# Kernel optimization log

Measured on AMD Instinct MI355X. Metric: run time of the kernel, lower is better.

Reference implementation:

```python
import jax, jax.numpy as jnp
import numpy as np

B, V, E = 8, 12288, 98304   # batch, nodes (healpix nside=32), edges (~8 nbrs/node)
FIN, FOUT, K = 256, 256, 4  # channels, Chebyshev order
EPS = 1e-5                  # BatchNorm1d eps


def setup_inputs() -> dict:
    key = jax.random.key(0)
    ks = jax.random.split(key, 5)
    x = jax.random.normal(ks[0], (B, V, FIN), jnp.float32)
    edge_src = jax.random.randint(ks[1], (E,), 0, V, dtype=jnp.int32)
    edge_dst = jax.random.randint(ks[2], (E,), 0, V, dtype=jnp.int32)
    edge_weight = jax.random.normal(ks[3], (E,), jnp.float32) * 0.3
    scale = (2.0 / (FIN * K)) ** 0.5  # kaiming-style init over K*Fin fan-in
    weight = jax.random.normal(ks[4], (K, FIN, FOUT), jnp.float32) * scale
    bias = jnp.zeros((FOUT,), jnp.float32)
    gamma = jnp.ones((FOUT,), jnp.float32)
    beta = jnp.zeros((FOUT,), jnp.float32)
    return {"x": x, "edge_weight": edge_weight, "weight": weight, "bias": bias,
            "gamma": gamma, "beta": beta, "edge_src": edge_src, "edge_dst": edge_dst}


def reference(x, edge_weight, weight, bias, gamma, beta, edge_src, edge_dst):
    # --- ConvCheb: Chebyshev polynomial recursion over sparse Laplacian ---
    xt = x.transpose(1, 0, 2)  # [V, B, Fin] (node-major for segment scatter)

    def lmul(y):  # sparse L @ y, y: [V, B, Fin]
        msg = edge_weight[:, None, None] * y[edge_src]          # [E, B, Fin]
        return jax.ops.segment_sum(msg, edge_dst, num_segments=V)

    xs = [xt]                                  # T_0(L) x = x
    if K > 1:
        xs.append(lmul(xt))                    # T_1(L) x = L x
    for _ in range(2, K):
        xs.append(2.0 * lmul(xs[-1]) - xs[-2])  # T_k = 2 L T_{k-1} - T_{k-2}
    xk = jnp.stack(xs)                         # [K, V, B, Fin]

    out = jnp.einsum('kvbi,kio->bvo', xk, weight) + bias  # [B, V, Fout]

    # --- BatchNorm1d over channels (training-mode batch stats over B,V) ---
    mean = out.mean(axis=(0, 1))
    var = out.var(axis=(0, 1))  # biased variance, as torch uses for normalization
    out = gamma * (out - mean) * jax.lax.rsqrt(var + EPS) + beta

    return jax.nn.relu(out)
```

## Files before the change

kernel.cpp:

```cpp
#include <hip/hip_runtime.h>

#define Vn    12288
#define En    98304
#define Mrows 98304

typedef unsigned short u16;
typedef u16   u16x8  __attribute__((ext_vector_type(8)));
typedef __bf16 bf16x8 __attribute__((ext_vector_type(8)));
typedef float f32x4  __attribute__((ext_vector_type(4)));

struct __align__(8) Edge { int s; float w; };

__device__ __forceinline__ float bf2f(u16 u) {
    union { float f; unsigned int i; } c; c.i = ((unsigned int)u) << 16; return c.f;
}
__device__ __forceinline__ u16 f2bf(float f) {
    union { float f; unsigned int i; } c; c.f = f;
    unsigned int r = c.i + 0x7fffu + ((c.i >> 16) & 1u);
    return (u16)(r >> 16);
}
__device__ __forceinline__ void load_lds16(const void* g, void* l) {
    __builtin_amdgcn_global_load_lds(
        (const __attribute__((address_space(1))) void*)g,
        (__attribute__((address_space(3))) void*)l, 16, 0, 0);
}

__global__ void cvt_k(const float* __restrict__ x, u16* __restrict__ xb) {
    int v = blockIdx.x;
    int t = threadIdx.x;
    int b = t >> 5, i = (t & 31) * 8;
    const float* p = x + ((size_t)b * Vn + v) * 256 + i;
    f32x4 a0 = __builtin_nontemporal_load((const f32x4*)p);
    f32x4 a1 = __builtin_nontemporal_load((const f32x4*)(p + 4));
    u16x8 r;
    #pragma unroll
    for (int j = 0; j < 4; ++j) { r[j] = f2bf(a0[j]); r[4 + j] = f2bf(a1[j]); }
    *(u16x8*)(xb + (size_t)v * 2048 + b * 256 + i) = r;
}

__global__ void wtrans_k(const float* __restrict__ w, u16* __restrict__ wt) {
    __shared__ u16 tile[32][1026];
    int o0 = blockIdx.x * 32;
    int t  = threadIdx.x;
    int lo = t & 31;
    int kr = t >> 5;
    for (int kk0 = 0; kk0 < 1024; kk0 += 8) {
        int kk = kk0 + kr;
        tile[lo][kk] = f2bf(w[(size_t)kk * 256 + o0 + lo]);
    }
    __syncthreads();
    for (int i = 0; i < 16; ++i) {
        int ch = i * 256 + t;
        int r = ch >> 7, c = ch & 127;
        u16x8 vv = *(const u16x8*)(&tile[r][c * 8]);
        *(u16x8*)(wt + (size_t)(o0 + r) * 1024 + c * 8) = vv;
    }
}

__global__ void count_k(const int* __restrict__ dst, int* __restrict__ counts) {
    int e = blockIdx.x * 256 + threadIdx.x;
    atomicAdd(&counts[dst[e]], 1);
}

__global__ void scan_k(const int* __restrict__ counts, int* __restrict__ row_start,
                       int* __restrict__ cursor) {
    __shared__ int par[1024];
    int t = threadIdx.x;
    int base = t * 12;
    int s = 0;
    #pragma unroll
    for (int i = 0; i < 12; ++i) s += counts[base + i];
    par[t] = s;
    __syncthreads();
    for (int off = 1; off < 1024; off <<= 1) {
        int v_ = (t >= off) ? par[t - off] : 0;
        __syncthreads();
        par[t] += v_;
        __syncthreads();
    }
    int run = (t == 0) ? 0 : par[t - 1];
    for (int i = 0; i < 12; ++i) {
        row_start[base + i] = run;
        cursor[base + i]    = run;
        run += counts[base + i];
    }
    if (t == 1023) row_start[Vn] = En;
}

__global__ void fill_k(const int* __restrict__ src, const int* __restrict__ dst,
                       const float* __restrict__ ew, int* __restrict__ cursor,
                       Edge* __restrict__ csr) {
    int e = blockIdx.x * 256 + threadIdx.x;
    int d = dst[e];
    int p = atomicAdd(&cursor[d], 1);
    Edge ed; ed.s = src[e]; ed.w = ew[e];
    csr[p] = ed;
}

template<int PREV>
__global__ __launch_bounds__(256)
void lmul_k(const u16* __restrict__ yb, const u16* __restrict__ prevb,
            u16* __restrict__ outb, const int* __restrict__ row_start,
            const Edge* __restrict__ csr)
{
    int slice = blockIdx.x & 7;
    int v     = (blockIdx.x >> 3) * 8 + (threadIdx.x >> 5);
    int t     = threadIdx.x & 31;
    int s0    = row_start[v];
    int cnt   = row_start[v + 1] - s0;
    size_t soff = (size_t)slice * 256 + (size_t)t * 8;
    float acc[8] = {0.f,0.f,0.f,0.f,0.f,0.f,0.f,0.f};
    for (int j0 = 0; j0 < cnt; j0 += 8) {
        int ss[8]; float ww[8];
        #pragma unroll
        for (int u = 0; u < 8; ++u) {
            int j = j0 + u;
            bool ok = j < cnt;
            Edge e = csr[s0 + (ok ? j : 0)];
            ss[u] = e.s; ww[u] = ok ? e.w : 0.f;
        }
        u16x8 g[8];
        #pragma unroll
        for (int u = 0; u < 8; ++u)
            g[u] = *(const u16x8*)(yb + (size_t)ss[u] * 2048 + soff);
        #pragma unroll
        for (int u = 0; u < 8; ++u)
            #pragma unroll
            for (int j8 = 0; j8 < 8; ++j8) acc[j8] += ww[u] * bf2f(g[u][j8]);
    }
    u16x8 r;
    if (PREV) {
        u16x8 pu = *(const u16x8*)(prevb + (size_t)v * 2048 + soff);
        #pragma unroll
        for (int j8 = 0; j8 < 8; ++j8) r[j8] = f2bf(2.0f * acc[j8] - bf2f(pu[j8]));
    } else {
        #pragma unroll
        for (int j8 = 0; j8 < 8; ++j8) r[j8] = f2bf(acc[j8]);
    }
    *(u16x8*)(outb + (size_t)v * 2048 + soff) = r;
}

__device__ __forceinline__ void stage_tile(const u16* __restrict__ Ak, int k0,
                                           const u16* __restrict__ wt, int kt,
                                           int m0, int tid, int wave,
                                           char* bufA, char* bufB)
{
    #pragma unroll
    for (int r = 0; r < 2; ++r) {
        int g  = r * 512 + tid;
        int ml = g >> 3;
        int c  = (g & 7) ^ (ml & 7);
        load_lds16(Ak + ((size_t)(m0 + ml)) * 256 + k0 + c * 8,
                   bufA + r * 8192 + wave * 1024);
    }
    #pragma unroll
    for (int r = 0; r < 4; ++r) {
        int g = r * 512 + tid;
        int o = g >> 3;
        int c = (g & 7) ^ (o & 7);
        load_lds16(wt + (size_t)o * 1024 + kt * 64 + c * 8,
                   bufB + r * 8192 + wave * 1024);
    }
}

__global__ __launch_bounds__(512)
void gemm_k(const u16* __restrict__ x0, const u16* __restrict__ x1,
            const u16* __restrict__ x2, const u16* __restrict__ x3,
            const u16* __restrict__ wt, const float* __restrict__ bias,
            u16* cbp, float* __restrict__ sums, float* __restrict__ sumsq)
{
    alignas(16) __shared__ char lds[147456];
    int tid  = threadIdx.x;
    int wave = tid >> 6;
    int lane = tid & 63;
    int m0   = blockIdx.x * 128;
    int wm   = wave & 1;
    int wn   = wave >> 1;

    f32x4 acc[4][4];
    #pragma unroll
    for (int a = 0; a < 4; ++a)
        #pragma unroll
        for (int b = 0; b < 4; ++b) acc[a][b] = (f32x4){0.f,0.f,0.f,0.f};

    stage_tile(x0, 0,  wt, 0, m0, tid, wave, (char*)lds,         (char*)lds + 16384);
    stage_tile(x0, 64, wt, 1, m0, tid, wave, (char*)lds + 49152, (char*)lds + 49152 + 16384);

    int cb = 0;
    int pb = 2;
    for (int t = 0; t < 16; ++t) {
        if (t < 15) asm volatile("s_waitcnt vmcnt(6) lgkmcnt(0)" ::: "memory");
        else        asm volatile("s_waitcnt vmcnt(0) lgkmcnt(0)" ::: "memory");
        __builtin_amdgcn_s_barrier();
        __builtin_amdgcn_sched_barrier(0);
        if (t < 14) {
            int kt = t + 2;
            int ks = kt >> 2;
            int k0 = (kt & 3) * 64;
            const u16* Ak = (ks == 0) ? x0 : (ks == 1) ? x1 : (ks == 2) ? x2 : x3;
            stage_tile(Ak, k0, wt, kt, m0, tid, wave,
                       (char*)lds + pb * 49152, (char*)lds + pb * 49152 + 16384);
        }
        const char* Ab = (const char*)lds + cb * 49152;
        const char* Bb = Ab + 16384;
        #pragma unroll
        for (int kstep = 0; kstep < 2; ++kstep) {
            int cidx = kstep * 4 + (lane >> 4);
            int row  = lane & 15;
            bf16x8 af[4], bfr[4];
            #pragma unroll
            for (int mt = 0; mt < 4; ++mt) {
                int m16 = wm * 64 + mt * 16 + row;
                af[mt] = *(const bf16x8*)(Ab + (size_t)(m16 * 8 + (cidx ^ (m16 & 7))) * 16);
            }
            #pragma unroll
            for (int nt = 0; nt < 4; ++nt) {
                int ol = wn * 64 + nt * 16 + row;
                bfr[nt] = *(const bf16x8*)(Bb + (size_t)(ol * 8 + (cidx ^ (ol & 7))) * 16);
            }
            __builtin_amdgcn_s_setprio(1);
            #pragma unroll
            for (int mt = 0; mt < 4; ++mt)
                #pragma unroll
                for (int nt = 0; nt < 4; ++nt)
                    acc[mt][nt] = __builtin_amdgcn_mfma_f32_16x16x32_bf16(
                        af[mt], bfr[nt], acc[mt][nt], 0, 0, 0);
            __builtin_amdgcn_s_setprio(0);
        }
        cb = (cb == 2) ? 0 : cb + 1;
        pb = (pb == 2) ? 0 : pb + 1;
    }

    __syncthreads();
    int crow = lane & 15, quad = lane >> 4;
    #pragma unroll
    for (int nt = 0; nt < 4; ++nt) {
        int o = wn * 64 + nt * 16 + crow;
        int c_o = o >> 3, o_in = (o & 7) * 2;
        float bv = bias[o];
        float ps = 0.f, pq = 0.f;
        #pragma unroll
        for (int mt = 0; mt < 4; ++mt) {
            #pragma unroll
            for (int r = 0; r < 4; ++r) {
                int ml = wm * 64 + mt * 16 + quad * 4 + r;
                u16 q = f2bf(acc[mt][nt][r] + bv);
                float vq = bf2f(q);
                *(u16*)(lds + (size_t)ml * 512 + (size_t)(c_o ^ (ml & 7)) * 16 + o_in) = q;
                ps += vq; pq += vq * vq;
            }
        }
        ps += __shfl_down(ps, 32, 64);  pq += __shfl_down(pq, 32, 64);
        ps += __shfl_down(ps, 16, 64);  pq += __shfl_down(pq, 16, 64);
        if (quad == 0) { atomicAdd(&sums[o], ps); atomicAdd(&sumsq[o], pq); }
    }
    __syncthreads();
    #pragma unroll
    for (int rr = 0; rr < 8; ++rr) {
        int ch = rr * 512 + tid;
        int ml = ch >> 5, c = ch & 31;
        u16x8 vv = *(const u16x8*)(lds + (size_t)ml * 512 + (size_t)(c ^ (ml & 7)) * 16);
        *(u16x8*)(cbp + (size_t)(m0 + ml) * 256 + c * 8) = vv;
    }
}

__global__ void bn_relu_k(const u16* __restrict__ cb, float* __restrict__ outp,
                          const float* __restrict__ sums, const float* __restrict__ sumsq,
                          const float* __restrict__ gamma, const float* __restrict__ beta) {
    __shared__ float ssc[256], ssh[256];
    int t = threadIdx.x;
    {
        const float invM = 1.0f / (float)Mrows;
        float mean = sums[t] * invM;
        float var  = sumsq[t] * invM - mean * mean;
        float sc   = gamma[t] * rsqrtf(var + 1e-5f);
        ssc[t] = sc;
        ssh[t] = beta[t] - mean * sc;
    }
    __syncthreads();
    size_t p = ((size_t)blockIdx.x * 256 + t) * 8;
    int o0 = (int)(p & 255);
    int m  = (int)(p >> 8);
    u16x8 v = __builtin_nontemporal_load((const u16x8*)(cb + p));
    float* dst = outp + ((size_t)((m & 7) * Vn + (m >> 3))) * 256 + o0;
    f32x4 a, c;
    #pragma unroll
    for (int i = 0; i < 4; ++i) {
        a[i] = fmaxf(bf2f(v[i])     * ssc[o0 + i]     + ssh[o0 + i],     0.f);
        c[i] = fmaxf(bf2f(v[4 + i]) * ssc[o0 + 4 + i] + ssh[o0 + 4 + i], 0.f);
    }
    __builtin_nontemporal_store(a, (f32x4*)dst);
    __builtin_nontemporal_store(c, (f32x4*)(dst + 4));
}

extern "C" void kernel_launch(void* const* d_in, const int* in_sizes, int n_in,
                              void* d_out, int out_size, void* d_ws, size_t ws_size,
                              hipStream_t stream) {
    const float* x     = (const float*)d_in[0];
    const float* ew    = (const float*)d_in[1];
    const float* w     = (const float*)d_in[2];
    const float* bias  = (const float*)d_in[3];
    const float* gamma = (const float*)d_in[4];
    const float* beta  = (const float*)d_in[5];
    const int*   esrc  = (const int*)d_in[6];
    const int*   edst  = (const int*)d_in[7];
    float* outp = (float*)d_out;
    char*  ws   = (char*)d_ws;

    u16*   xb        = (u16*)  (ws + 0);
    u16*   x1        = (u16*)  (ws + 50331648);
    u16*   x2        = (u16*)  (ws + 100663296);
    u16*   x3        = (u16*)  (ws + 150994944);
    u16*   wt        = (u16*)  (ws + 201326592);
    Edge*  csr       = (Edge*) (ws + 201850880);
    int*   counts    = (int*)  (ws + 202637312);
    int*   row_start = (int*)  (ws + 202686464);
    int*   cursor    = (int*)  (ws + 202736128);
    float* sums      = (float*)(ws + 202785280);
    float* sumsq     = (float*)(ws + 202786304);

    hipMemsetAsync(counts, 0, 49152, stream);
    hipMemsetAsync(sums, 0, 2048, stream);

    cvt_k<<<Vn, 256, 0, stream>>>(x, xb);
    wtrans_k<<<8, 256, 0, stream>>>(w, wt);
    count_k<<<384, 256, 0, stream>>>(edst, counts);
    scan_k<<<1, 1024, 0, stream>>>(counts, row_start, cursor);
    fill_k<<<384, 256, 0, stream>>>(esrc, edst, ew, cursor, csr);

    lmul_k<0><<<Vn, 256, 0, stream>>>(xb, nullptr, x1, row_start, csr);
    lmul_k<1><<<Vn, 256, 0, stream>>>(x1, xb,      x2, row_start, csr);
    lmul_k<1><<<Vn, 256, 0, stream>>>(x2, x1,      x3, row_start, csr);

    gemm_k<<<Mrows / 128, 512, 0, stream>>>(xb, x1, x2, x3, wt, bias,
                                            (u16*)x1, sums, sumsq);

    bn_relu_k<<<12288, 256, 0, stream>>>((const u16*)x1, outp, sums, sumsq, gamma, beta);
}
```

Before: 467.0 us.

## Fuse BatchNorm+ReLU into persistent GEMM kernel with a grid-wide barrier

The GEMM becomes persistent: 256 blocks each process three 128-row tiles and accumulate the channel sums as before. An atomic counter then acts as a grid-wide barrier, after which each block computes the BN scale and shift and applies BN+ReLU to its own tiles. This drops the separate bn_relu launch and lets the BN phase read its bf16 tiles while they are likely still cached. The barrier depends on all 256 blocks being resident at once, one per CU given the LDS use, or it will deadlock. The BN phase also cannot overlap with other blocks' GEMM work.

```diff
diff --git a/kernel.cpp b/kernel.cpp
--- a/kernel.cpp
+++ b/kernel.cpp
@@ -167,130 +167,151 @@
 void gemm_k(const u16* __restrict__ x0, const u16* __restrict__ x1,
             const u16* __restrict__ x2, const u16* __restrict__ x3,
             const u16* __restrict__ wt, const float* __restrict__ bias,
-            u16* cbp, float* __restrict__ sums, float* __restrict__ sumsq)
+            u16* cbp, float* __restrict__ sums, float* __restrict__ sumsq,
+            int* counter, const float* __restrict__ gamma,
+            const float* __restrict__ beta, float* __restrict__ outp)
 {
     alignas(16) __shared__ char lds[147456];
     int tid  = threadIdx.x;
     int wave = tid >> 6;
     int lane = tid & 63;
-    int m0   = blockIdx.x * 128;
     int wm   = wave & 1;
     int wn   = wave >> 1;
-
-    f32x4 acc[4][4];
-    #pragma unroll
-    for (int a = 0; a < 4; ++a)
-        #pragma unroll
-        for (int b = 0; b < 4; ++b) acc[a][b] = (f32x4){0.f,0.f,0.f,0.f};
-
-    stage_tile(x0, 0,  wt, 0, m0, tid, wave, (char*)lds,         (char*)lds + 16384);
-    stage_tile(x0, 64, wt, 1, m0, tid, wave, (char*)lds + 49152, (char*)lds + 49152 + 16384);
-
-    int cb = 0;
-    int pb = 2;
-    for (int t = 0; t < 16; ++t) {
-        if (t < 15) asm volatile("s_waitcnt vmcnt(6) lgkmcnt(0)" ::: "memory");
-        else        asm volatile("s_waitcnt vmcnt(0) lgkmcnt(0)" ::: "memory");
-        __builtin_amdgcn_s_barrier();
-        __builtin_amdgcn_sched_barrier(0);
-        if (t < 14) {
-            int kt = t + 2;
-            int ks = kt >> 2;
-            int k0 = (kt & 3) * 64;
-            const u16* Ak = (ks == 0) ? x0 : (ks == 1) ? x1 : (ks == 2) ? x2 : x3;
-            stage_tile(Ak, k0, wt, kt, m0, tid, wave,
-                       (char*)lds + pb * 49152, (char*)lds + pb * 49152 + 16384);
-        }
-        const char* Ab = (const char*)lds + cb * 49152;
-        const char* Bb = Ab + 16384;
-        #pragma unroll
-        for (int kstep = 0; kstep < 2; ++kstep) {
-            int cidx = kstep * 4 + (lane >> 4);
-            int row  = lane & 15;
-            bf16x8 af[4], bfr[4];
+    int crow = lane & 15, quad = lane >> 4;
+
+    for (int it = 0; it < 3; ++it) {
+        int m0 = (blockIdx.x * 3 + it) * 128;
+
+        f32x4 acc[4][4];
+        #pragma unroll
+        for (int a = 0; a < 4; ++a)
+            #pragma unroll
+            for (int b = 0; b < 4; ++b) acc[a][b] = (f32x4){0.f,0.f,0.f,0.f};
+
+        stage_tile(x0, 0,  wt, 0, m0, tid, wave, (char*)lds,         (char*)lds + 16384);
+        stage_tile(x0, 64, wt, 1, m0, tid, wave, (char*)lds + 49152, (char*)lds + 49152 + 16384);
+
+        int cb = 0;
+        int pb = 2;
+        for (int t = 0; t < 16; ++t) {
+            if (t < 15) asm volatile("s_waitcnt vmcnt(6) lgkmcnt(0)" ::: "memory");
+            else        asm volatile("s_waitcnt vmcnt(0) lgkmcnt(0)" ::: "memory");
+            __builtin_amdgcn_s_barrier();
+            __builtin_amdgcn_sched_barrier(0);
+            if (t < 14) {
+                int kt = t + 2;
+                int ks = kt >> 2;
+                int k0 = (kt & 3) * 64;
+                const u16* Ak = (ks == 0) ? x0 : (ks == 1) ? x1 : (ks == 2) ? x2 : x3;
+                stage_tile(Ak, k0, wt, kt, m0, tid, wave,
+                           (char*)lds + pb * 49152, (char*)lds + pb * 49152 + 16384);
+            }
+            const char* Ab = (const char*)lds + cb * 49152;
+            const char* Bb = Ab + 16384;
+            #pragma unroll
+            for (int kstep = 0; kstep < 2; ++kstep) {
+                int cidx = kstep * 4 + (lane >> 4);
+                int row  = lane & 15;
+                bf16x8 af[4], bfr[4];
+                #pragma unroll
+                for (int mt = 0; mt < 4; ++mt) {
+                    int m16 = wm * 64 + mt * 16 + row;
+                    af[mt] = *(const bf16x8*)(Ab + (size_t)(m16 * 8 + (cidx ^ (m16 & 7))) * 16);
+                }
+                #pragma unroll
+                for (int nt = 0; nt < 4; ++nt) {
+                    int ol = wn * 64 + nt * 16 + row;
+                    bfr[nt] = *(const bf16x8*)(Bb + (size_t)(ol * 8 + (cidx ^ (ol & 7))) * 16);
+                }
+                __builtin_amdgcn_s_setprio(1);
+                #pragma unroll
+                for (int mt = 0; mt < 4; ++mt)
+                    #pragma unroll
+                    for (int nt = 0; nt < 4; ++nt)
+                        acc[mt][nt] = __builtin_amdgcn_mfma_f32_16x16x32_bf16(
+                            af[mt], bfr[nt], acc[mt][nt], 0, 0, 0);
+                __builtin_amdgcn_s_setprio(0);
+            }
+            cb = (cb == 2) ? 0 : cb + 1;
+            pb = (pb == 2) ? 0 : pb + 1;
+        }
+
+        __syncthreads();
+        #pragma unroll
+        for (int nt = 0; nt < 4; ++nt) {
+            int o = wn * 64 + nt * 16 + crow;
+            int c_o = o >> 3, o_in = (o & 7) * 2;
+            float bv = bias[o];
+            float ps = 0.f, pq = 0.f;
             #pragma unroll
             for (int mt = 0; mt < 4; ++mt) {
-                int m16 = wm * 64 + mt * 16 + row;
-                af[mt] = *(const bf16x8*)(Ab + (size_t)(m16 * 8 + (cidx ^ (m16 & 7))) * 16);
+                #pragma unroll
+                for (int r = 0; r < 4; ++r) {
+                    int ml = wm * 64 + mt * 16 + quad * 4 + r;
+                    u16 q = f2bf(acc[mt][nt][r] + bv);
+                    float vq = bf2f(q);
+                    *(u16*)(lds + (size_t)ml * 512 + (size_t)(c_o ^ (ml & 7)) * 16 + o_in) = q;
+                    ps += vq; pq += vq * vq;
+                }
             }
-            #pragma unroll
-            for (int nt = 0; nt < 4; ++nt) {
-                int ol = wn * 64 + nt * 16 + row;
-                bfr[nt] = *(const bf16x8*)(Bb + (size_t)(ol * 8 + (cidx ^ (ol & 7))) * 16);
+            ps += __shfl_down(ps, 32, 64);  pq += __shfl_down(pq, 32, 64);
+            ps += __shfl_down(ps, 16, 64);  pq += __shfl_down(pq, 16, 64);
+            if (quad == 0) { atomicAdd(&sums[o], ps); atomicAdd(&sumsq[o], pq); }
+        }
+        __syncthreads();
+        #pragma unroll
+        for (int rr = 0; rr < 8; ++rr) {
+            int ch = rr * 512 + tid;
+            int ml = ch >> 5, c = ch & 31;
+            u16x8 vv = *(const u16x8*)(lds + (size_t)ml * 512 + (size_t)(c ^ (ml & 7)) * 16);
+            *(u16x8*)(cbp + (size_t)(m0 + ml) * 256 + c * 8) = vv;
+        }
+        __syncthreads();
+    }
+
+    __threadfence();
+    __syncthreads();
+    if (tid == 0) {
+        __hip_atomic_fetch_add(counter, 1, __ATOMIC_ACQ_REL, __HIP_MEMORY_SCOPE_AGENT);
+        while (__hip_atomic_load(counter, __ATOMIC_ACQUIRE, __HIP_MEMORY_SCOPE_AGENT) < 256)
+            __builtin_amdgcn_s_sleep(8);
+    }
+    __syncthreads();
+
+    float* ssc = (float*)lds;
+    float* ssh = (float*)(lds + 1024);
+    if (tid < 256) {
+        const float invM = 1.0f / (float)Mrows;
+        float s = __hip_atomic_load(&sums[tid],  __ATOMIC_RELAXED, __HIP_MEMORY_SCOPE_AGENT);
+        float q = __hip_atomic_load(&sumsq[tid], __ATOMIC_RELAXED, __HIP_MEMORY_SCOPE_AGENT);
+        float mean = s * invM;
+        float var  = q * invM - mean * mean;
+        float sc   = gamma[tid] * rsqrtf(var + 1e-5f);
+        ssc[tid] = sc;
+        ssh[tid] = beta[tid] - mean * sc;
+    }
+    __syncthreads();
+
+    for (int it = 0; it < 3; ++it) {
+        int m0 = (blockIdx.x * 3 + it) * 128;
+        #pragma unroll
+        for (int i = 0; i < 8; ++i) {
+            int ch = i * 512 + tid;
+            int ml = ch >> 5, c = ch & 31;
+            int m  = m0 + ml;
+            int o0 = c * 8;
+            u16x8 v = *(const u16x8*)(cbp + (size_t)m * 256 + o0);
+            float* dst = outp + ((size_t)((m & 7) * Vn + (m >> 3))) * 256 + o0;
+            f32x4 a, cc;
+            #pragma unroll
+            for (int j = 0; j < 4; ++j) {
+                a[j]  = fmaxf(bf2f(v[j])     * ssc[o0 + j]     + ssh[o0 + j],     0.f);
+                cc[j] = fmaxf(bf2f(v[4 + j]) * ssc[o0 + 4 + j] + ssh[o0 + 4 + j], 0.f);
             }
-            __builtin_amdgcn_s_setprio(1);
-            #pragma unroll
-            for (int mt = 0; mt < 4; ++mt)
-                #pragma unroll
-                for (int nt = 0; nt < 4; ++nt)
-                    acc[mt][nt] = __builtin_amdgcn_mfma_f32_16x16x32_bf16(
-                        af[mt], bfr[nt], acc[mt][nt], 0, 0, 0);
-            __builtin_amdgcn_s_setprio(0);
-        }
-        cb = (cb == 2) ? 0 : cb + 1;
-        pb = (pb == 2) ? 0 : pb + 1;
-    }
-
-    __syncthreads();
-    int crow = lane & 15, quad = lane >> 4;
-    #pragma unroll
-    for (int nt = 0; nt < 4; ++nt) {
-        int o = wn * 64 + nt * 16 + crow;
-        int c_o = o >> 3, o_in = (o & 7) * 2;
-        float bv = bias[o];
-        float ps = 0.f, pq = 0.f;
-        #pragma unroll
-        for (int mt = 0; mt < 4; ++mt) {
-            #pragma unroll
-            for (int r = 0; r < 4; ++r) {
-                int ml = wm * 64 + mt * 16 + quad * 4 + r;
-                u16 q = f2bf(acc[mt][nt][r] + bv);
-                float vq = bf2f(q);
-                *(u16*)(lds + (size_t)ml * 512 + (size_t)(c_o ^ (ml & 7)) * 16 + o_in) = q;
-                ps += vq; pq += vq * vq;
-            }
-        }
-        ps += __shfl_down(ps, 32, 64);  pq += __shfl_down(pq, 32, 64);
-        ps += __shfl_down(ps, 16, 64);  pq += __shfl_down(pq, 16, 64);
-        if (quad == 0) { atomicAdd(&sums[o], ps); atomicAdd(&sumsq[o], pq); }
-    }
-    __syncthreads();
-    #pragma unroll
-    for (int rr = 0; rr < 8; ++rr) {
-        int ch = rr * 512 + tid;
-        int ml = ch >> 5, c = ch & 31;
-        u16x8 vv = *(const u16x8*)(lds + (size_t)ml * 512 + (size_t)(c ^ (ml & 7)) * 16);
-        *(u16x8*)(cbp + (size_t)(m0 + ml) * 256 + c * 8) = vv;
-    }
-}
-
-__global__ void bn_relu_k(const u16* __restrict__ cb, float* __restrict__ outp,
-                          const float* __restrict__ sums, const float* __restrict__ sumsq,
-                          const float* __restrict__ gamma, const float* __restrict__ beta) {
-    __shared__ float ssc[256], ssh[256];
-    int t = threadIdx.x;
-    {
-        const float invM = 1.0f / (float)Mrows;
-        float mean = sums[t] * invM;
-        float var  = sumsq[t] * invM - mean * mean;
-        float sc   = gamma[t] * rsqrtf(var + 1e-5f);
-        ssc[t] = sc;
-        ssh[t] = beta[t] - mean * sc;
-    }
-    __syncthreads();
-    size_t p = ((size_t)blockIdx.x * 256 + t) * 8;
-    int o0 = (int)(p & 255);
-    int m  = (int)(p >> 8);
-    u16x8 v = __builtin_nontemporal_load((const u16x8*)(cb + p));
-    float* dst = outp + ((size_t)((m & 7) * Vn + (m >> 3))) * 256 + o0;
-    f32x4 a, c;
-    #pragma unroll
-    for (int i = 0; i < 4; ++i) {
-        a[i] = fmaxf(bf2f(v[i])     * ssc[o0 + i]     + ssh[o0 + i],     0.f);
-        c[i] = fmaxf(bf2f(v[4 + i]) * ssc[o0 + 4 + i] + ssh[o0 + 4 + i], 0.f);
-    }
-    __builtin_nontemporal_store(a, (f32x4*)dst);
-    __builtin_nontemporal_store(c, (f32x4*)(dst + 4));
+            __builtin_nontemporal_store(a,  (f32x4*)dst);
+            __builtin_nontemporal_store(cc, (f32x4*)(dst + 4));
+        }
+    }
 }
 
 extern "C" void kernel_launch(void* const* d_in, const int* in_sizes, int n_in,
@@ -318,9 +339,10 @@
     int*   cursor    = (int*)  (ws + 202736128);
     float* sums      = (float*)(ws + 202785280);
     float* sumsq     = (float*)(ws + 202786304);
+    int*   counter   = (int*)  (ws + 202787328);
 
     hipMemsetAsync(counts, 0, 49152, stream);
-    hipMemsetAsync(sums, 0, 2048, stream);
+    hipMemsetAsync(sums, 0, 2052, stream);
 
     cvt_k<<<Vn, 256, 0, stream>>>(x, xb);
     wtrans_k<<<8, 256, 0, stream>>>(w, wt);
@@ -332,8 +354,7 @@
     lmul_k<1><<<Vn, 256, 0, stream>>>(x1, xb,      x2, row_start, csr);
     lmul_k<1><<<Vn, 256, 0, stream>>>(x2, x1,      x3, row_start, csr);
 
-    gemm_k<<<Mrows / 128, 512, 0, stream>>>(xb, x1, x2, x3, wt, bias,
-                                            (u16*)x1, sums, sumsq);
-
-    bn_relu_k<<<12288, 256, 0, stream>>>((const u16*)x1, outp, sums, sumsq, gamma, beta);
-}
+    gemm_k<<<256, 512, 0, stream>>>(xb, x1, x2, x3, wt, bias,
+                                    (u16*)x1, sums, sumsq, counter,
+                                    gamma, beta, outp);
+}
```

Result: slower. 550.5 us (+17.9%).
